# Performance work log

Hardware: AMD Instinct MI355X
Metric: run time of the kernel (lower is better)

## Reference

```python
import jax, jax.numpy as jnp
import numpy as np

B, T, IN, H, OUT = 32, 512, 50, 512, 66
DIGITS = 5          # total_digits -> 6 softmax blocks of width 11
EPS = 0.01          # ACT halting threshold epsilon
MAX_PONDER = 10     # max ponder steps per timestep (fixed for jit)


def setup_inputs() -> dict:
    key = jax.random.key(0)
    ks = jax.random.split(key, 6)
    s_in = 1.0 / np.sqrt(IN + 1)
    s_h = 1.0 / np.sqrt(H)
    return {
        "x": jax.random.normal(ks[0], (B, T, IN), jnp.float32),
        # LSTM cell over input augmented with the ACT first-step flag (IN+1)
        "W_ih": jax.random.normal(ks[1], (4 * H, IN + 1), jnp.float32) * s_in,
        "W_hh": jax.random.normal(ks[2], (4 * H, H), jnp.float32) * s_h,
        "b": jnp.zeros((4 * H,), jnp.float32),
        "W_out": jax.random.normal(ks[3], (OUT, H), jnp.float32) * s_h,
        "b_out": jnp.zeros((OUT,), jnp.float32),
        "W_halt": jax.random.normal(ks[4], (H,), jnp.float32) * s_h,
        "b_halt": jnp.ones((), jnp.float32),
    }


def _lstm_cell(x_aug, h, c, W_ih, W_hh, b):
    g = x_aug @ W_ih.T + h @ W_hh.T + b          # [B, 4H]
    i, f, gg, o = jnp.split(g, 4, axis=-1)
    c = jax.nn.sigmoid(f) * c + jax.nn.sigmoid(i) * jnp.tanh(gg)
    h = jax.nn.sigmoid(o) * jnp.tanh(c)
    return h, c


def _act_lstm(x, W_ih, W_hh, b, W_out, b_out, W_halt, b_halt):
    Bb, Tt, _ = x.shape
    h0 = jnp.zeros((Bb, H), x.dtype)
    c0 = jnp.zeros((Bb, H), x.dtype)

    def time_step(carry, x_t):
        h, c = carry

        def ponder_step(pc, n):
            ph, pcell, cum, acc_h, acc_c, acc_y, n_upd, rem, done = pc
            flag = jnp.where(n == 0, 1.0, 0.0).astype(x_t.dtype)
            x_aug = jnp.concatenate(
                [x_t, jnp.broadcast_to(flag, (Bb, 1))], axis=-1)
            h2, c2 = _lstm_cell(x_aug, ph, pcell, W_ih, W_hh, b)
            y = h2 @ W_out.T + b_out                    # [B, OUT]
            halt = jax.nn.sigmoid(h2 @ W_halt + b_halt)  # [B]
            is_last = n == (MAX_PONDER - 1)
            halted = ((cum + halt) > (1.0 - EPS)) | is_last
            p = jnp.where(done, 0.0, jnp.where(halted, 1.0 - cum, halt))
            acc_h = acc_h + p[:, None] * h2
            acc_c = acc_c + p[:, None] * c2
            acc_y = acc_y + p[:, None] * y
            n_upd = n_upd + jnp.where(done, 0.0, 1.0)
            rem = rem + jnp.where(done | ~halted, 0.0, 1.0 - cum)
            cum = cum + jnp.where(done, 0.0, halt)
            done = done | halted
            return (h2, c2, cum, acc_h, acc_c, acc_y, n_upd, rem, done), None

        zb = jnp.zeros((Bb,), x.dtype)
        init = (h, c, zb,
                jnp.zeros((Bb, H), x.dtype), jnp.zeros((Bb, H), x.dtype),
                jnp.zeros((Bb, OUT), x.dtype), zb, zb,
                jnp.zeros((Bb,), bool))
        (_, _, _, wh, wc, wy, n_upd, rem, _), _ = jax.lax.scan(
            ponder_step, init, jnp.arange(MAX_PONDER))
        return (wh, wc), (wy, n_upd + rem)

    _, (ys, p) = jax.lax.scan(time_step, (h0, c0), jnp.swapaxes(x, 0, 1))
    out = jnp.swapaxes(ys, 0, 1)   # [B, T, OUT]
    p = jnp.swapaxes(p, 0, 1)      # [B, T] ponder cost
    return out, p


def reference(x, W_ih, W_hh, b, W_out, b_out, W_halt, b_halt):
    out, p = _act_lstm(x, W_ih, W_hh, b, W_out, b_out, W_halt, b_halt)
    Bb, Tt, _ = out.shape
    # per-segment softmax: 6 blocks of width 11 along the feature axis
    out = jax.nn.softmax(out.reshape(Bb, Tt, DIGITS + 1, 11), axis=-1)
    out = out.reshape(Bb, Tt, OUT)
    return out, p
```

## Files before the change

### kernel.cpp

```cpp
#include <hip/hip_runtime.h>
#include <stdint.h>
#include <stddef.h>


#define NBLK 256

#define WS_NEED_BYTES 38434816ull

__device__ __forceinline__ float sigmf(float v) { return 1.0f / (1.0f + expf(-v)); }

__device__ __forceinline__ unsigned load_llc_u(const unsigned* p) {
  unsigned v;
  asm volatile("global_load_dword %0, %1, off sc0 sc1\ns_waitcnt vmcnt(0)"
               : "=&v"(v) : "v"(p) : "memory");
  return v;
}

__global__ void prep_k(const float* __restrict__ W_ih, const float* __restrict__ W_hh,
                       float* __restrict__ Wp, float* __restrict__ W_iT,
                       float* __restrict__ comm) {
  int idx = blockIdx.x * 256 + threadIdx.x;
  if (idx < 1048576) {
    int kl = idx & 3, c = (idx >> 2) & 63, k4 = (idx >> 8) & 127, r = idx >> 15;
    int row = (c & 3) * 512 + 16 * r + (c >> 2);
    Wp[idx] = W_hh[(size_t)row * 512 + 4 * k4 + kl];
  }
  int i2 = idx - 1048576;
  if (i2 >= 0 && i2 < 104448) {
    int col = i2 & 2047, k = i2 >> 11;
    int g = col & 3, j = col >> 2;
    W_iT[i2] = W_ih[(size_t)((g << 9) + j) * 51 + k];
  }
  int i3 = idx - 1153024;
  if (i3 >= 0 && i3 < 40960) comm[i3] = 0.0f;
}

__global__ void prep2_k(const float* __restrict__ W_out, float* __restrict__ W_oT) {
  int i = blockIdx.x * 256 + threadIdx.x;
  if (i < 33792) {
    int k = i / 66, o = i - k * 66;
    W_oT[i] = W_out[(size_t)o * 512 + k];
  }
}

__global__ void __launch_bounds__(256)
act_main(const float* __restrict__ x, const float* __restrict__ bvec,
         const float* __restrict__ W_halt, const float* __restrict__ b_halt,
         const float* __restrict__ Wp, const float* __restrict__ W_iT,
         float* __restrict__ comm, float* __restrict__ wh,
         float* __restrict__ p_out) {
  extern __shared__ __align__(16) float wl[];
  __shared__ float hst[2052];
  __shared__ float pacc[1024];
  __shared__ float xg2[256];
  __shared__ float hps[256];
  __shared__ float pubf[80];
  __shared__ float S_p[4];
  __shared__ int S_flag[1];

  const int tid = threadIdx.x, bid = blockIdx.x;
  const int gid = bid >> 5, r = bid & 31;
  const int c = tid & 63, w = tid >> 6, lane = tid & 63;
  const int jj = tid >> 2, bo = tid & 3;
  const int ch = lane >> 2, b2 = lane & 3;

  {
    const float* wsrc = Wp + (size_t)r * 32768;
    for (int i = tid; i < 8192; i += 256)
      *(float4*)(wl + i * 4) = *(const float4*)(wsrc + i * 4);
  }

  const float bh = b_halt[0];
  const int cg = 64 * r + c;
  const float bs = bvec[(c & 3) * 512 + 16 * r + (c >> 2)];
  const float wfc = W_iT[50 * 2048 + cg];

  const int pub_off = (tid / 15) * 16 + (tid % 15);
  const int sp_off = (lane / 5) * 80 + (lane % 5) * 16 + 15;

#define MKH(GW, DST) do { const int _q=(GW)/80, _o=(GW)%80, _li=_o>>4, _po=_o&15; \
    const int _pi = _li*15 + _po; \
    DST = ((_po < 15) && (_pi < 64)) ? (w*512 + _q*64 + _pi) : 2048; } while (0)
  int hA0,hA1,hA2,hA3,hB0,hB1,hB2,hB3;
  int hC0=2048,hC1=2048,hC2=2048,hC3=2048;
  MKH(4*lane+0,hA0); MKH(4*lane+1,hA1); MKH(4*lane+2,hA2); MKH(4*lane+3,hA3);
  MKH(256+4*lane+0,hB0); MKH(256+4*lane+1,hB1);
  MKH(256+4*lane+2,hB2); MKH(256+4*lane+3,hB3);
  if (lane < 32) {
    MKH(512+4*lane+0,hC0); MKH(512+4*lane+1,hC1);
    MKH(512+4*lane+2,hC2); MKH(512+4*lane+3,hC3);
  }
#undef MKH

  float gAcc = 0.f, gxc, gxn = 0.f;
  {
    gxc = bs;
    const float* xr = x + (size_t)(gid * 4 + w) * 512 * 50;
    for (int k = 0; k < 50; ++k) gxc = fmaf(xr[k], W_iT[k * 2048 + cg], gxc);
  }
  float cS = 0.f, hprev = 0.f, acc_h = 0.f, acc_c = 0.f;
  float cum = 0.f, nupd = 0.f, rem = 0.f;
  int mydone = 0;

  int t = 0, n = 0, first = 1;
  unsigned ph = 0;
  long pollbud = 8000000L;
  __syncthreads();

  while (true) {
    float val, cin = 0.f;
    if (first) {
      val = gxc + wfc;
      first = 0;
    } else {
      const unsigned par_rd = (ph & 1u) ^ 1u;
      const float* cb = comm + (size_t)(par_rd * 256u + gid * 32 + 8 * w) * 80;
      {
        const unsigned* stp = (const unsigned*)cb + sp_off;
        while (true) {
          unsigned sv = 0u;
          if (lane < 40) sv = load_llc_u(stp);
          if (__ballot((lane < 40) ? (sv >= ph) : 1) == ~0ull) break;
          if (--pollbud < 0) break;
          __builtin_amdgcn_s_sleep(1);
        }
      }
      float4 vA, vB, vC;
      asm volatile("global_load_dwordx4 %0, %1, off sc0 sc1"
                   : "=v"(vA) : "v"(cb + 4 * lane) : "memory");
      asm volatile("global_load_dwordx4 %0, %1, off sc0 sc1"
                   : "=v"(vB) : "v"(cb + 256 + 4 * lane) : "memory");
      if (lane < 32)
        asm volatile("global_load_dwordx4 %0, %1, off sc0 sc1"
                     : "=v"(vC) : "v"(cb + 512 + 4 * lane) : "memory");
      if (n == 0) {
        const int tn = (t + 1 > 511) ? 511 : t + 1;
        gxn = bs;
        const float* xr = x + ((size_t)(gid * 4 + w) * 512 + tn) * 50;
        for (int k = 0; k < 50; ++k) gxn = fmaf(xr[k], W_iT[k * 2048 + cg], gxn);
      }
      asm volatile("s_waitcnt vmcnt(0)" ::: "memory");
      hst[hA0] = vA.x; hst[hA1] = vA.y; hst[hA2] = vA.z; hst[hA3] = vA.w;
      hst[hB0] = vB.x; hst[hB1] = vB.y; hst[hB2] = vB.z; hst[hB3] = vB.w;
      if (lane < 32) {
        hst[hC0] = vC.x; hst[hC1] = vC.y; hst[hC2] = vC.z; hst[hC3] = vC.w;
      }

      {
        const float* wb = wl + w * 8192 + c * 4;
        const float* hb = hst + w * 512;
        float a0 = 0.f, a1 = 0.f, a2 = 0.f, a3 = 0.f;
        #pragma unroll 8
        for (int i = 0; i < 32; ++i) {
          const float4 wv = *(const float4*)(wb + i * 256);
          const float4 h0 = *(const float4*)(hb + i * 16);
          const float4 h1 = *(const float4*)(hb + i * 16 + 4);
          const float4 h2v = *(const float4*)(hb + i * 16 + 8);
          const float4 h3 = *(const float4*)(hb + i * 16 + 12);
          a0 = fmaf(wv.x, h0.x, a0); a1 = fmaf(wv.x, h0.y, a1);
          a2 = fmaf(wv.x, h0.z, a2); a3 = fmaf(wv.x, h0.w, a3);
          a0 = fmaf(wv.y, h1.x, a0); a1 = fmaf(wv.y, h1.y, a1);
          a2 = fmaf(wv.y, h1.z, a2); a3 = fmaf(wv.y, h1.w, a3);
          a0 = fmaf(wv.z, h2v.x, a0); a1 = fmaf(wv.z, h2v.y, a1);
          a2 = fmaf(wv.z, h2v.z, a2); a3 = fmaf(wv.z, h2v.w, a3);
          a0 = fmaf(wv.w, h3.x, a0); a1 = fmaf(wv.w, h3.y, a1);
          a2 = fmaf(wv.w, h3.z, a2); a3 = fmaf(wv.w, h3.w, a3);
        }
        float4 pv; pv.x = a0; pv.y = a1; pv.z = a2; pv.w = a3;
        *(float4*)(pacc + w * 256 + c * 4) = pv;
      }
      {
        float hp = 0.f;
        #pragma unroll
        for (int i = 0; i < 8; ++i) {
          const int k = 128 * w + ch + 16 * i;
          hp = fmaf(hst[k * 4 + b2], W_halt[k], hp);
        }
        hps[tid] = hp;
      }
      __syncthreads();

      const float g = pacc[c * 4 + w] + pacc[256 + c * 4 + w] +
                      pacc[512 + c * 4 + w] + pacc[768 + c * 4 + w];
      if (tid < 64) {
        float s = hps[tid] + hps[tid + 64] + hps[tid + 128] + hps[tid + 192];
        s += __shfl_xor(s, 4);  s += __shfl_xor(s, 8);
        s += __shfl_xor(s, 16); s += __shfl_xor(s, 32);
        int vote = 1;
        if (tid < 4) {
          const float halt = sigmf(s + bh);
          const int done = mydone;
          const int halted = ((cum + halt) > 0.99f) || (n == 9);
          S_p[tid] = done ? 0.f : (halted ? (1.f - cum) : halt);
          nupd += done ? 0.f : 1.f;
          rem += (done || !halted) ? 0.f : (1.f - cum);
          cum += done ? 0.f : halt;
          mydone = done | halted;
          vote = mydone;
        }
        const unsigned long long bal = __ballot(vote);
        if (tid == 0) S_flag[0] = (bal == ~0ull) ? 1 : 0;
      }
      __syncthreads();

      const int alldone = S_flag[0];
      const float p = S_p[w];
      gAcc = fmaf(p, g, gAcc);
      if (tid < 64) {
        const float po = S_p[bo];
        acc_h = fmaf(po, hprev, acc_h);
        acc_c = fmaf(po, cS, acc_c);
      }
      if (alldone) {
        if (tid < 64) {
          wh[(size_t)t * 16384 + (size_t)(gid * 4 + bo) * 512 + 16 * r + jj] = acc_h;
          cin = acc_c;
          acc_h = 0.f; acc_c = 0.f;
        }
        if (r == 0 && tid < 4)
          p_out[(size_t)(gid * 4 + tid) * 512 + t] = nupd + rem;
        if (tid < 4) { cum = 0.f; nupd = 0.f; rem = 0.f; mydone = 0; }
        val = gxn + wfc + gAcc;
        gAcc = 0.f; gxc = gxn;
        t += 1; n = 0;
        if (t == 512) break;
      } else {
        if (tid < 64) cin = cS;
        val = gxc + g;
        n += 1;
      }
    }

    xg2[c * 4 + w] = val;
    __syncthreads();
    if (tid < 64) {
      const float gi = xg2[16 * jj + 0 + bo];
      const float gf = xg2[16 * jj + 4 + bo];
      const float gg = xg2[16 * jj + 8 + bo];
      const float go = xg2[16 * jj + 12 + bo];
      const float c_new = sigmf(gf) * cin + sigmf(gi) * tanhf(gg);
      const float h_new = sigmf(go) * tanhf(c_new);
      cS = c_new; hprev = h_new;
      pubf[pub_off] = h_new;
      if (tid < 5) pubf[tid * 16 + 15] = __uint_as_float(ph + 1u);
    }
    asm volatile("s_waitcnt lgkmcnt(0)" ::: "memory");
    __builtin_amdgcn_sched_barrier(0);
    if (tid < 40) {
      const float2 pv = *(const float2*)&pubf[2 * tid];
      float* cp = comm + (size_t)((ph & 1u) * 256u + gid * 32 + r) * 80 + 2 * tid;
      asm volatile("global_store_dwordx2 %0, %1, off sc0 sc1"
                   :: "v"(cp), "v"(pv) : "memory");
    }
    ph += 1;
  }
}

__global__ void __launch_bounds__(256)
epi_k(const float* __restrict__ wh, const float* __restrict__ W_oT,
      const float* __restrict__ b_out, float* __restrict__ out) {
  __shared__ float hl[4][512];
  __shared__ float yl[4][66];
  const int tid = threadIdx.x, pair = tid >> 6, lane = tid & 63;
  const int bt = blockIdx.x * 4 + pair;
  const int b = bt >> 9, t = bt & 511;
  const float* hsrc = wh + (size_t)t * 16384 + (size_t)b * 512;
  *(float4*)&hl[pair][lane * 8] = *(const float4*)(hsrc + lane * 8);
  *(float4*)&hl[pair][lane * 8 + 4] = *(const float4*)(hsrc + lane * 8 + 4);
  __syncthreads();
  if (lane < 33) {
    const int o = lane * 2;
    float y0 = b_out[o], y1 = b_out[o + 1];
    const float* hp_ = hl[pair];
    #pragma unroll 8
    for (int k = 0; k < 512; ++k) {
      const float h = hp_[k];
      const float2 wv = *(const float2*)(W_oT + k * 66 + o);
      y0 = fmaf(h, wv.x, y0);
      y1 = fmaf(h, wv.y, y1);
    }
    yl[pair][o] = y0; yl[pair][o + 1] = y1;
  }
  __syncthreads();
  if (tid < 24) {
    const int pr = tid / 6, g = tid - pr * 6;
    const int bt2 = blockIdx.x * 4 + pr;
    const float* yp = &yl[pr][g * 11];
    float m = yp[0];
    for (int u = 1; u < 11; ++u) m = fmaxf(m, yp[u]);
    float e[11], ssum = 0.f;
    for (int u = 0; u < 11; ++u) { e[u] = expf(yp[u] - m); ssum += e[u]; }
    const float inv = 1.0f / ssum;
    float* op = out + (size_t)bt2 * 66 + g * 11;
    for (int u = 0; u < 11; ++u) op[u] = e[u] * inv;
  }
}

extern "C" void kernel_launch(void* const* d_in, const int* in_sizes, int n_in,
                              void* d_out, int out_size, void* d_ws, size_t ws_size,
                              hipStream_t stream) {
  (void)in_sizes; (void)n_in; (void)out_size;
  const float* x      = (const float*)d_in[0];
  const float* W_ih   = (const float*)d_in[1];
  const float* W_hh   = (const float*)d_in[2];
  const float* bvec   = (const float*)d_in[3];
  const float* W_out  = (const float*)d_in[4];
  const float* b_out  = (const float*)d_in[5];
  const float* W_halt = (const float*)d_in[6];
  const float* b_halt = (const float*)d_in[7];
  float* out = (float*)d_out;
  float* ws  = (float*)d_ws;

  if (ws_size < (size_t)WS_NEED_BYTES) return;

  float* wh   = ws;
  float* comm = ws + 8388608;
  float* Wp   = ws + 8429568;
  float* W_iT = ws + 9478144;
  float* W_oT = ws + 8429568;
  float* p_out = out + 1081344;

  static int s_attr = 0;
  if (!s_attr) {
    (void)hipFuncSetAttribute((const void*)act_main,
                              hipFuncAttributeMaxDynamicSharedMemorySize, 131072);
    s_attr = 1;
  }

  hipLaunchKernelGGL(prep_k, dim3(4664), dim3(256), 0, stream,
                     W_ih, W_hh, Wp, W_iT, comm);

  void* args[9];
  args[0] = (void*)&x;      args[1] = (void*)&bvec;  args[2] = (void*)&W_halt;
  args[3] = (void*)&b_halt; args[4] = (void*)&Wp;    args[5] = (void*)&W_iT;
  args[6] = (void*)&comm;   args[7] = (void*)&wh;    args[8] = (void*)&p_out;
  hipError_t ce = hipLaunchCooperativeKernel((void*)act_main, dim3(NBLK), dim3(256),
                                             args, 131072, stream);
  if (ce != hipSuccess) {
    hipLaunchKernelGGL(act_main, dim3(NBLK), dim3(256), 131072, stream,
                       x, bvec, W_halt, b_halt, Wp, W_iT, comm, wh, p_out);
  }

  hipLaunchKernelGGL(prep2_k, dim3(132), dim3(256), 0, stream, W_out, W_oT);
  hipLaunchKernelGGL(epi_k, dim3(4096), dim3(256), 0, stream, wh, W_oT, b_out, out);
}
```

Baseline: 7.030 ms.

## Fuse flag polling with data loads and compute halting redundantly per thread

Each thread now reads its h payload directly, checking per-slot sequence tags embedded in the payload. This replaces the separate poll on status words followed by a second load, and drops the sleep in the poll loop. The halt-score reduction now uses wave shuffles into a 16-entry shared array. Every thread recomputes the ACT halting state for all four batch rows, which removes one __syncthreads and the shared S_p/S_flag broadcast per ponder step. In exchange the poll loop issues more memory traffic, every thread does redundant sigmoid work, and the poll budget is lowered.

```diff
diff --git a/kernel.cpp b/kernel.cpp
--- a/kernel.cpp
+++ b/kernel.cpp
@@ -8,13 +8,6 @@
 #define WS_NEED_BYTES 38434816ull
 
 __device__ __forceinline__ float sigmf(float v) { return 1.0f / (1.0f + expf(-v)); }
-
-__device__ __forceinline__ unsigned load_llc_u(const unsigned* p) {
-  unsigned v;
-  asm volatile("global_load_dword %0, %1, off sc0 sc1\ns_waitcnt vmcnt(0)"
-               : "=&v"(v) : "v"(p) : "memory");
-  return v;
-}
 
 __global__ void prep_k(const float* __restrict__ W_ih, const float* __restrict__ W_hh,
                        float* __restrict__ Wp, float* __restrict__ W_iT,
@@ -53,10 +46,8 @@
   __shared__ float hst[2052];
   __shared__ float pacc[1024];
   __shared__ float xg2[256];
-  __shared__ float hps[256];
+  __shared__ float hps2[16];
   __shared__ float pubf[80];
-  __shared__ float S_p[4];
-  __shared__ int S_flag[1];
 
   const int tid = threadIdx.x, bid = blockIdx.x;
   const int gid = bid >> 5, r = bid & 31;
@@ -76,7 +67,6 @@
   const float wfc = W_iT[50 * 2048 + cg];
 
   const int pub_off = (tid / 15) * 16 + (tid % 15);
-  const int sp_off = (lane / 5) * 80 + (lane % 5) * 16 + 15;
 
 #define MKH(GW, DST) do { const int _q=(GW)/80, _o=(GW)%80, _li=_o>>4, _po=_o&15; \
     const int _pi = _li*15 + _po; \
@@ -99,12 +89,13 @@
     for (int k = 0; k < 50; ++k) gxc = fmaf(xr[k], W_iT[k * 2048 + cg], gxc);
   }
   float cS = 0.f, hprev = 0.f, acc_h = 0.f, acc_c = 0.f;
-  float cum = 0.f, nupd = 0.f, rem = 0.f;
-  int mydone = 0;
+  float cum0 = 0.f, cum1 = 0.f, cum2 = 0.f, cum3 = 0.f;
+  int doneM = 0;
+  float nupd = 0.f, rem = 0.f;
 
   int t = 0, n = 0, first = 1;
   unsigned ph = 0;
-  long pollbud = 8000000L;
+  long pollbud = 2000000L;
   __syncthreads();
 
   while (true) {
@@ -115,31 +106,36 @@
     } else {
       const unsigned par_rd = (ph & 1u) ^ 1u;
       const float* cb = comm + (size_t)(par_rd * 256u + gid * 32 + 8 * w) * 80;
+      float4 vA, vB, vC;
+      vC.x = vC.y = vC.z = vC.w = 0.f;
       {
-        const unsigned* stp = (const unsigned*)cb + sp_off;
+        const float* pA = cb + 4 * lane;
+        const float* pB = cb + 256 + 4 * lane;
+        const float* pC = cb + 512 + 4 * lane;
         while (true) {
-          unsigned sv = 0u;
-          if (lane < 40) sv = load_llc_u(stp);
-          if (__ballot((lane < 40) ? (sv >= ph) : 1) == ~0ull) break;
+          asm volatile("global_load_dwordx4 %0, %1, off sc0 sc1"
+                       : "=v"(vA) : "v"(pA) : "memory");
+          asm volatile("global_load_dwordx4 %0, %1, off sc0 sc1"
+                       : "=v"(vB) : "v"(pB) : "memory");
+          if (lane < 32)
+            asm volatile("global_load_dwordx4 %0, %1, off sc0 sc1"
+                         : "=v"(vC) : "v"(pC) : "memory");
+          asm volatile("s_waitcnt vmcnt(0)" ::: "memory");
+          int ok = 1;
+          if ((lane & 3) == 3) {
+            ok = (__float_as_uint(vA.w) >= ph) && (__float_as_uint(vB.w) >= ph);
+            if (lane < 32) ok = ok && (__float_as_uint(vC.w) >= ph);
+          }
+          if (__ballot(ok) == ~0ull) break;
           if (--pollbud < 0) break;
-          __builtin_amdgcn_s_sleep(1);
         }
       }
-      float4 vA, vB, vC;
-      asm volatile("global_load_dwordx4 %0, %1, off sc0 sc1"
-                   : "=v"(vA) : "v"(cb + 4 * lane) : "memory");
-      asm volatile("global_load_dwordx4 %0, %1, off sc0 sc1"
-                   : "=v"(vB) : "v"(cb + 256 + 4 * lane) : "memory");
-      if (lane < 32)
-        asm volatile("global_load_dwordx4 %0, %1, off sc0 sc1"
-                     : "=v"(vC) : "v"(cb + 512 + 4 * lane) : "memory");
       if (n == 0) {
         const int tn = (t + 1 > 511) ? 511 : t + 1;
         gxn = bs;
         const float* xr = x + ((size_t)(gid * 4 + w) * 512 + tn) * 50;
         for (int k = 0; k < 50; ++k) gxn = fmaf(xr[k], W_iT[k * 2048 + cg], gxn);
       }
-      asm volatile("s_waitcnt vmcnt(0)" ::: "memory");
       hst[hA0] = vA.x; hst[hA1] = vA.y; hst[hA2] = vA.z; hst[hA3] = vA.w;
       hst[hB0] = vB.x; hst[hB1] = vB.y; hst[hB2] = vB.z; hst[hB3] = vB.w;
       if (lane < 32) {
@@ -176,38 +172,45 @@
           const int k = 128 * w + ch + 16 * i;
           hp = fmaf(hst[k * 4 + b2], W_halt[k], hp);
         }
-        hps[tid] = hp;
+        hp += __shfl_xor(hp, 4);  hp += __shfl_xor(hp, 8);
+        hp += __shfl_xor(hp, 16); hp += __shfl_xor(hp, 32);
+        if (lane < 4) hps2[w * 4 + lane] = hp;
       }
       __syncthreads();
 
       const float g = pacc[c * 4 + w] + pacc[256 + c * 4 + w] +
                       pacc[512 + c * 4 + w] + pacc[768 + c * 4 + w];
-      if (tid < 64) {
-        float s = hps[tid] + hps[tid + 64] + hps[tid + 128] + hps[tid + 192];
-        s += __shfl_xor(s, 4);  s += __shfl_xor(s, 8);
-        s += __shfl_xor(s, 16); s += __shfl_xor(s, 32);
-        int vote = 1;
-        if (tid < 4) {
-          const float halt = sigmf(s + bh);
-          const int done = mydone;
-          const int halted = ((cum + halt) > 0.99f) || (n == 9);
-          S_p[tid] = done ? 0.f : (halted ? (1.f - cum) : halt);
-          nupd += done ? 0.f : 1.f;
-          rem += (done || !halted) ? 0.f : (1.f - cum);
-          cum += done ? 0.f : halt;
-          mydone = done | halted;
-          vote = mydone;
-        }
-        const unsigned long long bal = __ballot(vote);
-        if (tid == 0) S_flag[0] = (bal == ~0ull) ? 1 : 0;
-      }
-      __syncthreads();
-
-      const int alldone = S_flag[0];
-      const float p = S_p[w];
+      const float d0 = hps2[0] + hps2[4] + hps2[8] + hps2[12];
+      const float d1 = hps2[1] + hps2[5] + hps2[9] + hps2[13];
+      const float d2 = hps2[2] + hps2[6] + hps2[10] + hps2[14];
+      const float d3 = hps2[3] + hps2[7] + hps2[11] + hps2[15];
+      const float e0 = sigmf(d0 + bh), e1 = sigmf(d1 + bh);
+      const float e2 = sigmf(d2 + bh), e3 = sigmf(d3 + bh);
+      const int last = (n == 9) ? 1 : 0;
+      const int ha0 = (((cum0 + e0) > 0.99f) | last);
+      const int ha1 = (((cum1 + e1) > 0.99f) | last);
+      const int ha2 = (((cum2 + e2) > 0.99f) | last);
+      const int ha3 = (((cum3 + e3) > 0.99f) | last);
+      const float q0 = (doneM & 1) ? 0.f : (ha0 ? (1.f - cum0) : e0);
+      const float q1 = (doneM & 2) ? 0.f : (ha1 ? (1.f - cum1) : e1);
+      const float q2 = (doneM & 4) ? 0.f : (ha2 ? (1.f - cum2) : e2);
+      const float q3 = (doneM & 8) ? 0.f : (ha3 ? (1.f - cum3) : e3);
+      if (tid < 4) {
+        const int dmy = (doneM >> tid) & 1;
+        const int hamy = (tid == 0) ? ha0 : (tid == 1) ? ha1 : (tid == 2) ? ha2 : ha3;
+        const float cmy = (tid == 0) ? cum0 : (tid == 1) ? cum1 : (tid == 2) ? cum2 : cum3;
+        nupd += dmy ? 0.f : 1.f;
+        rem += (dmy || !hamy) ? 0.f : (1.f - cmy);
+      }
+      cum0 += (doneM & 1) ? 0.f : e0;  cum1 += (doneM & 2) ? 0.f : e1;
+      cum2 += (doneM & 4) ? 0.f : e2;  cum3 += (doneM & 8) ? 0.f : e3;
+      doneM |= ha0 | (ha1 << 1) | (ha2 << 2) | (ha3 << 3);
+      const int alldone = (doneM == 15);
+
+      const float p = (w == 0) ? q0 : (w == 1) ? q1 : (w == 2) ? q2 : q3;
       gAcc = fmaf(p, g, gAcc);
       if (tid < 64) {
-        const float po = S_p[bo];
+        const float po = (bo == 0) ? q0 : (bo == 1) ? q1 : (bo == 2) ? q2 : q3;
         acc_h = fmaf(po, hprev, acc_h);
         acc_c = fmaf(po, cS, acc_c);
       }
@@ -219,7 +222,8 @@
         }
         if (r == 0 && tid < 4)
           p_out[(size_t)(gid * 4 + tid) * 512 + t] = nupd + rem;
-        if (tid < 4) { cum = 0.f; nupd = 0.f; rem = 0.f; mydone = 0; }
+        nupd = 0.f; rem = 0.f;
+        cum0 = cum1 = cum2 = cum3 = 0.f; doneM = 0;
         val = gxn + wfc + gAcc;
         gAcc = 0.f; gxc = gxn;
         t += 1; n = 0;
```

Measured after the change: 7.297 ms. 1.04x slower.
